# Kernel optimization log

Measured on AMD Instinct MI355X. Metric: run time of the kernel, lower is better.

## Reference

```python
import jax, jax.numpy as jnp
import numpy as np
from jax import lax

COS_BASIS_NO = 24
SCALE = 6.0
SHIFT = 1.0


def make_kern_basis(T_no):
    # [24, T_no] raised-cosine log-time basis, matching the torch loop exactly
    i = jnp.arange(COS_BASIS_NO, dtype=jnp.float32)
    phi = (jnp.pi / 2.0) * i                                  # [24]
    x = jnp.arange(T_no, dtype=jnp.float32)
    raw = SCALE * jnp.log(x + SHIFT + 1e-7)                   # [T_no]
    basis = 0.5 * jnp.cos(raw[None, :] - phi[:, None]) + 0.5  # [24, T_no]
    inside = (raw[None, :] >= phi[:, None] - jnp.pi) & (raw[None, :] <= phi[:, None] + jnp.pi)
    return jnp.where(inside, basis, 0.0)


def causal_grouped_conv(x, kern, sub_no, T_no):
    # x: [B, sub_no, T], kern: [sub_no*hid, T_no] (already flipped like torch)
    # left-pad T_no-1 zeros == the torch zero-padded buffer; cross-correlation
    rhs = kern[:, None, :]  # OIH with I=1 per group
    return lax.conv_general_dilated(
        x, rhs, window_strides=(1,), padding=[(T_no - 1, 0)],
        feature_group_count=sub_no,
        dimension_numbers=("NCH", "OIH", "NCH"))


def setup_inputs() -> dict:
    key = jax.random.key(0)
    ks = jax.random.split(key, 10)
    B, T_data = 8, 5000
    sub_no, E_no, I_no, T_no, hid_no = 20, 2000, 200, 400, 16
    inp = {
        "S_e": jax.random.uniform(ks[0], (B, T_data, E_no), dtype=jnp.float32),
        "S_i": jax.random.uniform(ks[1], (B, T_data, I_no), dtype=jnp.float32),
        "E_scale": jnp.zeros((E_no,), jnp.float32),
        "I_scale": jnp.zeros((I_no,), jnp.float32),
        "W_e_layer1": jax.random.normal(ks[2], (sub_no * hid_no, COS_BASIS_NO), jnp.float32) * 0.01,
        "W_i_layer1": jax.random.normal(ks[3], (sub_no * hid_no, COS_BASIS_NO), jnp.float32) * 0.01,
        "W_layer2": jnp.full((sub_no, hid_no), -1.0, jnp.float32),
        "b_layer1": jnp.zeros((sub_no * hid_no,), jnp.float32),
        "C_syn_e_raw": jax.random.normal(ks[4], (sub_no, E_no), jnp.float32) * 0.01,
        "C_syn_i_raw": jax.random.normal(ks[5], (sub_no, I_no), jnp.float32) * 0.01,
        "V_o": jnp.zeros((1,), jnp.float32),
        "temp": jnp.asarray(1.0, jnp.float32),
        "T_no": T_no,
        "test": 1,
    }
    return inp


def reference(S_e, S_i, E_scale, I_scale, W_e_layer1, W_i_layer1, W_layer2,
              b_layer1, C_syn_e_raw, C_syn_i_raw, V_o, temp, T_no, test):
    sub_no = C_syn_e_raw.shape[0]
    hid_no = W_layer2.shape[1]
    B, T_data, _ = S_e.shape

    if test:
        C_syn_e = jax.nn.softmax(C_syn_e_raw / temp, axis=0)
        C_syn_i = jax.nn.softmax(C_syn_i_raw / temp, axis=0)
    else:
        eps = 1e-8
        ku, kv = jax.random.split(jax.random.key(42))
        u_e = jax.random.uniform(ku, C_syn_e_raw.shape, dtype=C_syn_e_raw.dtype)
        u_i = jax.random.uniform(kv, C_syn_i_raw.shape, dtype=C_syn_i_raw.dtype)
        g_e = -jnp.log(-jnp.log(u_e + eps) + eps)
        g_i = -jnp.log(-jnp.log(u_i + eps) + eps)
        C_syn_e = jax.nn.softmax((C_syn_e_raw + g_e) / temp, axis=0)
        C_syn_i = jax.nn.softmax((C_syn_i_raw + g_i) / temp, axis=0)

    # scale synapses and project onto subunits: [B,T,E] x [E,sub] -> [B,T,sub]
    syn_e = jnp.einsum("bte,se->bts", S_e * jnp.exp(E_scale)[None, None, :], C_syn_e)
    syn_i = jnp.einsum("bti,si->bts", S_i * jnp.exp(I_scale)[None, None, :], C_syn_i)

    kern_basis = make_kern_basis(T_no)                        # [24, T_no]
    ke = jnp.flip(W_e_layer1 @ kern_basis, axis=1)            # [sub*hid, T_no]
    ki = jnp.flip(W_i_layer1 @ kern_basis, axis=1)

    xe = jnp.transpose(syn_e, (0, 2, 1))                      # [B, sub, T]
    xi = jnp.transpose(syn_i, (0, 2, 1))
    conv_e = causal_grouped_conv(xe, ke, sub_no, T_no)        # [B, sub*hid, T]
    conv_i = causal_grouped_conv(xi, ki, sub_no, T_no)
    layer1 = jnp.tanh(conv_e + conv_i + b_layer1[None, :, None])

    # grouped 1x1 conv == per-subunit weighted reduction over hid
    h = layer1.reshape(B, sub_no, hid_no, T_data)
    sub_out = jnp.einsum("bshT,sh->bTs", h, jnp.exp(W_layer2))  # [B, T, sub]
    final = jnp.sum(sub_out, axis=-1) + V_o                    # [B, T]
    return final, sub_out, C_syn_e, C_syn_i
```

## Files before the change

kernel.cpp:

```cpp
#include <hip/hip_runtime.h>
#include <math.h>

#define PI_F 3.14159265358979323846f
#define BSTRIDE 404

__global__ __launch_bounds__(256) void prep_kernel(
    const float* __restrict__ Ce_raw, const float* __restrict__ Ci_raw,
    const float* __restrict__ Escale, const float* __restrict__ Iscale,
    const float* __restrict__ temp,
    float* __restrict__ CsT_e, float* __restrict__ CsT_i,
    float* __restrict__ basis,
    float* __restrict__ outCe, float* __restrict__ outCi)
{
    int id = blockIdx.x * 256 + threadIdx.x;
    if (id < 2000) {
        int e = id;
        float t = temp[0];
        float v[20];
        float m = -1e30f;
        #pragma unroll
        for (int s = 0; s < 20; ++s) { v[s] = Ce_raw[s * 2000 + e] / t; m = fmaxf(m, v[s]); }
        float sum = 0.f;
        #pragma unroll
        for (int s = 0; s < 20; ++s) { v[s] = expf(v[s] - m); sum += v[s]; }
        float inv = 1.f / sum;
        float sc = expf(Escale[e]);
        #pragma unroll
        for (int s = 0; s < 20; ++s) {
            float p = v[s] * inv;
            outCe[s * 2000 + e] = p;
            CsT_e[e * 20 + s] = p * sc;
        }
    } else if (id < 2200) {
        int e = id - 2000;
        float t = temp[0];
        float v[20];
        float m = -1e30f;
        #pragma unroll
        for (int s = 0; s < 20; ++s) { v[s] = Ci_raw[s * 200 + e] / t; m = fmaxf(m, v[s]); }
        float sum = 0.f;
        #pragma unroll
        for (int s = 0; s < 20; ++s) { v[s] = expf(v[s] - m); sum += v[s]; }
        float inv = 1.f / sum;
        float sc = expf(Iscale[e]);
        #pragma unroll
        for (int s = 0; s < 20; ++s) {
            float p = v[s] * inv;
            outCi[s * 200 + e] = p;
            CsT_i[e * 20 + s] = p * sc;
        }
    } else if (id < 2200 + 24 * BSTRIDE) {
        int idx = id - 2200;
        int j = idx / BSTRIDE, d = idx - j * BSTRIDE;
        float val = 0.f;
        if (d < 400) {
            float raw = 6.0f * logf((float)d + 1.0f + 1e-7f);
            float ph = (PI_F * 0.5f) * (float)j;
            if (raw >= ph - PI_F && raw <= ph + PI_F) val = 0.5f * cosf(raw - ph) + 0.5f;
        }
        basis[idx] = val;
    } else if (id < 11896 + 48) {
        int row = 2000 + (id - 11896);
        #pragma unroll
        for (int s = 0; s < 20; ++s) CsT_e[row * 20 + s] = 0.f;
    } else if (id < 11944 + 56) {
        int row = 200 + (id - 11944);
        #pragma unroll
        for (int s = 0; s < 20; ++s) CsT_i[row * 20 + s] = 0.f;
    }
}

template <int NCHUNK>
__global__ __launch_bounds__(256) void syn_kernel(
    const float* __restrict__ S, const float* __restrict__ CsT,
    float* __restrict__ syn, int Eno)
{
    __shared__ float4 tile[64 * 33];
    float* red = reinterpret_cast<float*>(tile);
    const int tid = threadIdx.x;
    const int lane = tid & 63;
    const int w = __builtin_amdgcn_readfirstlane(tid >> 6);
    const int r0 = blockIdx.x * 64;

    float acc[20];
    #pragma unroll
    for (int s = 0; s < 20; ++s) acc[s] = 0.f;

    const int frow = tid >> 5, fcol = tid & 31;

    auto issue = [&](int ch, float4 (&v)[8]) {
        const int ebase = ch * 128;
        #pragma unroll
        for (int i = 0; i < 8; ++i) {
            int row = frow + i * 8;
            int e0 = ebase + fcol * 4;
            v[i] = make_float4(0.f, 0.f, 0.f, 0.f);
            if (e0 + 4 <= Eno)
                v[i] = *reinterpret_cast<const float4*>(S + (size_t)(r0 + row) * Eno + e0);
        }
    };
    auto put = [&](float4 (&v)[8]) {
        #pragma unroll
        for (int i = 0; i < 8; ++i)
            tile[(frow + i * 8) * 33 + fcol] = v[i];
    };

    float4 nx[8];
    issue(0, nx);
    put(nx);

    for (int ch = 0; ch < NCHUNK; ++ch) {
        __syncthreads();
        if (ch + 1 < NCHUNK) issue(ch + 1, nx);

        const int ebase = ch * 128;
        const float4* crow = reinterpret_cast<const float4*>(CsT + (size_t)(ebase + w * 32) * 20);
        #pragma unroll
        for (int c4 = 0; c4 < 8; ++c4) {
            float4 v = tile[lane * 33 + w * 8 + c4];
            const float4* ct = crow + c4 * 20;
            float vv[4] = {v.x, v.y, v.z, v.w};
            #pragma unroll
            for (int q = 0; q < 4; ++q) {
                float sv = vv[q];
                #pragma unroll
                for (int c5 = 0; c5 < 5; ++c5) {
                    float4 cc = ct[q * 5 + c5];
                    acc[c5 * 4 + 0] = fmaf(sv, cc.x, acc[c5 * 4 + 0]);
                    acc[c5 * 4 + 1] = fmaf(sv, cc.y, acc[c5 * 4 + 1]);
                    acc[c5 * 4 + 2] = fmaf(sv, cc.z, acc[c5 * 4 + 2]);
                    acc[c5 * 4 + 3] = fmaf(sv, cc.w, acc[c5 * 4 + 3]);
                }
            }
        }
        __syncthreads();
        if (ch + 1 < NCHUNK) put(nx);
    }

    #pragma unroll
    for (int s = 0; s < 20; ++s) red[(w * 64 + lane) * 21 + s] = acc[s];
    __syncthreads();

    #pragma unroll
    for (int i = 0; i < 5; ++i) {
        int p = tid + i * 256;
        int row = p & 63, s = p >> 6;
        float a = red[(0 * 64 + row) * 21 + s] + red[(1 * 64 + row) * 21 + s]
                + red[(2 * 64 + row) * 21 + s] + red[(3 * 64 + row) * 21 + s];
        int r = r0 + row;
        int b = r / 5000, t = r - b * 5000;
        syn[((size_t)b * 20 + s) * 5000 + t] = a;
    }
}

__device__ const int CJ_LO[24] = {0,0,0,0,0,0,0,0,0,4,4,8,12,16,20,28,36,48,64,84,108,140,184,240};
__device__ const int CJ_NB[24] = {1,1,1,1,2,2,3,3,4,4,5,6,7,9,12,15,19,25,31,41,53,65,54,40};

__device__ __forceinline__ int phys4(int g) {
    return (g & ~15) | ((g >> 1) & 7) | ((g & 1) << 3);
}

__global__ __launch_bounds__(128) void conv_kernel(
    const float* __restrict__ syn_e, const float* __restrict__ syn_i,
    const float* __restrict__ basis,
    const float* __restrict__ W_e, const float* __restrict__ W_i,
    const float* __restrict__ b1, const float* __restrict__ W2,
    float* __restrict__ sub_out)
{
    __shared__ float4 win4[16 + 464];
    float4* wbase = win4 + 16;
    float2* win2 = reinterpret_cast<float2*>(wbase);
    const int tid = threadIdx.x;
    const int tile = blockIdx.x, s = blockIdx.y, bz = blockIdx.z;
    const int t0 = tile * 512;

    const float* se = syn_e + ((size_t)bz * 20 + s) * 5000;
    const float* si = syn_i + ((size_t)bz * 20 + s) * 5000;
    for (int l = tid; l < 920; l += 128) {
        int t = t0 - 404 + l;
        float ve = 0.f, vi = 0.f;
        if ((unsigned)t < 5000u) { ve = se[t]; vi = si[t]; }
        int g = l >> 1;
        win2[2 * phys4(g) + (l & 1)] = make_float2(ve, vi);
    }
    __syncthreads();

    float z[16][4];
    #pragma unroll
    for (int h = 0; h < 16; ++h) {
        float bv = b1[s * 16 + h];
        #pragma unroll
        for (int k = 0; k < 4; ++k) z[h][k] = bv;
    }

    const int base = 4 * tid + 400;

    for (int j = 0; j < 24; ++j) {
        const float4* bj4 = reinterpret_cast<const float4*>(basis + j * BSTRIDE);
        const int lo = CJ_LO[j];
        const int nb = CJ_NB[j];
        const int co = lo >> 2;
        float be0 = 0.f, be1 = 0.f, be2 = 0.f, be3 = 0.f;
        float bi0 = 0.f, bi1 = 0.f, bi2 = 0.f, bi3 = 0.f;

        auto body = [&](const float4& V0, const float4& V1,
                        const float4& V2, const float4& V3, const float4& c) {
            be0 = fmaf(c.x, V2.x, be0); bi0 = fmaf(c.x, V2.y, bi0);
            be1 = fmaf(c.x, V2.z, be1); bi1 = fmaf(c.x, V2.w, bi1);
            be2 = fmaf(c.x, V3.x, be2); bi2 = fmaf(c.x, V3.y, bi2);
            be3 = fmaf(c.x, V3.z, be3); bi3 = fmaf(c.x, V3.w, bi3);
            be0 = fmaf(c.y, V1.z, be0); bi0 = fmaf(c.y, V1.w, bi0);
            be1 = fmaf(c.y, V2.x, be1); bi1 = fmaf(c.y, V2.y, bi1);
            be2 = fmaf(c.y, V2.z, be2); bi2 = fmaf(c.y, V2.w, bi2);
            be3 = fmaf(c.y, V3.x, be3); bi3 = fmaf(c.y, V3.y, bi3);
            be0 = fmaf(c.z, V1.x, be0); bi0 = fmaf(c.z, V1.y, bi0);
            be1 = fmaf(c.z, V1.z, be1); bi1 = fmaf(c.z, V1.w, bi1);
            be2 = fmaf(c.z, V2.x, be2); bi2 = fmaf(c.z, V2.y, bi2);
            be3 = fmaf(c.z, V2.z, be3); bi3 = fmaf(c.z, V2.w, bi3);
            be0 = fmaf(c.w, V0.z, be0); bi0 = fmaf(c.w, V0.w, bi0);
            be1 = fmaf(c.w, V1.x, be1); bi1 = fmaf(c.w, V1.y, bi1);
            be2 = fmaf(c.w, V1.z, be2); bi2 = fmaf(c.w, V1.w, bi2);
            be3 = fmaf(c.w, V2.x, be3); bi3 = fmaf(c.w, V2.y, bi3);
        };

        const int g0 = (base - lo) >> 1;
        auto LP = [&](int n, float4& lo4, float4& hi4) {
            int p = phys4(g0 - 2 * n);
            lo4 = wbase[p]; hi4 = wbase[p + 8];
        };

        float4 A0, A1, B0, B1, C0, C1, D0, D1;
        float4 E0, E1, F0, F1, G0, G1, H0, H1;
        LP(-1, A0, A1); LP(0, B0, B1); LP(1, C0, C1); LP(2, D0, D1);
        float4 cB = bj4[co], cC = bj4[co + 1], cD = bj4[co + 2];

        int bb = 0;
        while (bb + 8 <= nb) {
            LP(bb + 3, E0, E1); float4 cE = bj4[co + bb + 3];
            body(B0, B1, A0, A1, cB);
            LP(bb + 4, F0, F1); float4 cF = bj4[co + bb + 4];
            body(C0, C1, B0, B1, cC);
            LP(bb + 5, G0, G1); float4 cG = bj4[co + bb + 5];
            body(D0, D1, C0, C1, cD);
            LP(bb + 6, H0, H1); float4 cH = bj4[co + bb + 6];
            body(E0, E1, D0, D1, cE);
            LP(bb + 7, A0, A1); float4 cI = bj4[co + bb + 7];
            body(F0, F1, E0, E1, cF);
            LP(bb + 8, B0, B1); cB = bj4[co + bb + 8];
            body(G0, G1, F0, F1, cG);
            LP(bb + 9, C0, C1); cC = bj4[co + bb + 9];
            body(H0, H1, G0, G1, cH);
            LP(bb + 10, D0, D1); cD = bj4[co + bb + 10];
            body(A0, A1, H0, H1, cI);
            bb += 8;
        }
        int r = nb - bb;
        if (r > 0) { body(B0, B1, A0, A1, cB);
          if (r > 1) { body(C0, C1, B0, B1, cC);
            if (r > 2) { body(D0, D1, C0, C1, cD);
              if (r > 3) { LP(bb + 3, E0, E1); float4 cE = bj4[co + bb + 3];
                body(E0, E1, D0, D1, cE);
                if (r > 4) { LP(bb + 4, F0, F1); float4 cF = bj4[co + bb + 4];
                  body(F0, F1, E0, E1, cF);
                  if (r > 5) { LP(bb + 5, G0, G1); float4 cG = bj4[co + bb + 5];
                    body(G0, G1, F0, F1, cG);
                    if (r > 6) { LP(bb + 6, H0, H1); float4 cH = bj4[co + bb + 6];
                      body(H0, H1, G0, G1, cH); } } } } } } }

        #pragma unroll
        for (int h = 0; h < 16; ++h) {
            float we = W_e[(s * 16 + h) * 24 + j];
            float wi = W_i[(s * 16 + h) * 24 + j];
            z[h][0] = fmaf(we, be0, fmaf(wi, bi0, z[h][0]));
            z[h][1] = fmaf(we, be1, fmaf(wi, bi1, z[h][1]));
            z[h][2] = fmaf(we, be2, fmaf(wi, bi2, z[h][2]));
            z[h][3] = fmaf(we, be3, fmaf(wi, bi3, z[h][3]));
        }
    }

    float w2v[16];
    #pragma unroll
    for (int h = 0; h < 16; ++h) w2v[h] = __expf(W2[s * 16 + h]);

    #pragma unroll
    for (int k = 0; k < 4; ++k) {
        int t = t0 + 4 * tid + k;
        if (t < 5000) {
            float acc = 0.f;
            #pragma unroll
            for (int h = 0; h < 16; ++h) {
                float e2 = __expf(2.0f * z[h][k]);
                float th = 1.0f - 2.0f / (e2 + 1.0f);
                acc = fmaf(w2v[h], th, acc);
            }
            sub_out[((size_t)bz * 5000 + t) * 20 + s] = acc;
        }
    }
}

__global__ __launch_bounds__(256) void final_kernel(
    const float* __restrict__ sub_out, const float* __restrict__ V_o,
    float* __restrict__ fin)
{
    int r = blockIdx.x * 256 + threadIdx.x;
    if (r < 40000) {
        const float* p = sub_out + (size_t)r * 20;
        float a = V_o[0];
        #pragma unroll
        for (int s = 0; s < 20; ++s) a += p[s];
        fin[r] = a;
    }
}

extern "C" void kernel_launch(void* const* d_in, const int* in_sizes, int n_in,
                              void* d_out, int out_size, void* d_ws, size_t ws_size,
                              hipStream_t stream)
{
    const float* S_e     = (const float*)d_in[0];
    const float* S_i     = (const float*)d_in[1];
    const float* E_scale = (const float*)d_in[2];
    const float* I_scale = (const float*)d_in[3];
    const float* W_e     = (const float*)d_in[4];
    const float* W_i     = (const float*)d_in[5];
    const float* W2      = (const float*)d_in[6];
    const float* b1      = (const float*)d_in[7];
    const float* Ce_raw  = (const float*)d_in[8];
    const float* Ci_raw  = (const float*)d_in[9];
    const float* V_o     = (const float*)d_in[10];
    const float* temp    = (const float*)d_in[11];

    float* out     = (float*)d_out;
    float* fin     = out;
    float* sub_out = out + 40000;
    float* outCe   = out + 840000;
    float* outCi   = out + 880000;

    float* ws    = (float*)d_ws;
    float* CsT_e = ws;
    float* CsT_i = ws + 40960;
    float* basis = ws + 46080;
    float* syn_e = ws + 55776;
    float* syn_i = ws + 855776;

    prep_kernel<<<47, 256, 0, stream>>>(Ce_raw, Ci_raw, E_scale, I_scale, temp,
                                        CsT_e, CsT_i, basis, outCe, outCi);
    syn_kernel<16><<<625, 256, 0, stream>>>(S_e, CsT_e, syn_e, 2000);
    syn_kernel<2><<<625, 256, 0, stream>>>(S_i, CsT_i, syn_i, 200);
    conv_kernel<<<dim3(10, 20, 8), 128, 0, stream>>>(syn_e, syn_i, basis,
                                                     W_e, W_i, b1, W2, sub_out);
    final_kernel<<<157, 256, 0, stream>>>(sub_out, V_o, fin);
}
```

Baseline: 292.6 us.

## Restructure synapse projection as per-wave 4-row dot products with blocked coefficient layout

The synapse projection kernel no longer stages S tiles through shared memory with block-wide syncs. Each wave now handles 4 time rows: lanes stride over the input dimension and read coalesced scalars of S, then finish with a shuffle reduction across the wave. The prep kernel writes the softmax coefficients in a lane-interleaved float4 layout so each lane loads its 20 coefficients with vector loads. This drops the LDS traffic and barriers, at the cost of 80 accumulators per thread, a 6-step shuffle reduction per output, and scalar rather than float4 global loads of S.

```diff
diff --git a/kernel.cpp b/kernel.cpp
--- a/kernel.cpp
+++ b/kernel.cpp
@@ -8,7 +8,7 @@
     const float* __restrict__ Ce_raw, const float* __restrict__ Ci_raw,
     const float* __restrict__ Escale, const float* __restrict__ Iscale,
     const float* __restrict__ temp,
-    float* __restrict__ CsT_e, float* __restrict__ CsT_i,
+    float4* __restrict__ CbE, float4* __restrict__ CbI,
     float* __restrict__ basis,
     float* __restrict__ outCe, float* __restrict__ outCi)
 {
@@ -25,11 +25,16 @@
         for (int s = 0; s < 20; ++s) { v[s] = expf(v[s] - m); sum += v[s]; }
         float inv = 1.f / sum;
         float sc = expf(Escale[e]);
-        #pragma unroll
-        for (int s = 0; s < 20; ++s) {
-            float p = v[s] * inv;
-            outCe[s * 2000 + e] = p;
-            CsT_e[e * 20 + s] = p * sc;
+        int bi = (e >> 6) * 5, ln = e & 63;
+        #pragma unroll
+        for (int s4 = 0; s4 < 5; ++s4) {
+            float p0 = v[s4*4+0] * inv, p1 = v[s4*4+1] * inv;
+            float p2 = v[s4*4+2] * inv, p3 = v[s4*4+3] * inv;
+            outCe[(s4*4+0) * 2000 + e] = p0;
+            outCe[(s4*4+1) * 2000 + e] = p1;
+            outCe[(s4*4+2) * 2000 + e] = p2;
+            outCe[(s4*4+3) * 2000 + e] = p3;
+            CbE[(bi + s4) * 64 + ln] = make_float4(p0*sc, p1*sc, p2*sc, p3*sc);
         }
     } else if (id < 2200) {
         int e = id - 2000;
@@ -43,11 +48,16 @@
         for (int s = 0; s < 20; ++s) { v[s] = expf(v[s] - m); sum += v[s]; }
         float inv = 1.f / sum;
         float sc = expf(Iscale[e]);
-        #pragma unroll
-        for (int s = 0; s < 20; ++s) {
-            float p = v[s] * inv;
-            outCi[s * 200 + e] = p;
-            CsT_i[e * 20 + s] = p * sc;
+        int bi = (e >> 6) * 5, ln = e & 63;
+        #pragma unroll
+        for (int s4 = 0; s4 < 5; ++s4) {
+            float p0 = v[s4*4+0] * inv, p1 = v[s4*4+1] * inv;
+            float p2 = v[s4*4+2] * inv, p3 = v[s4*4+3] * inv;
+            outCi[(s4*4+0) * 200 + e] = p0;
+            outCi[(s4*4+1) * 200 + e] = p1;
+            outCi[(s4*4+2) * 200 + e] = p2;
+            outCi[(s4*4+3) * 200 + e] = p3;
+            CbI[(bi + s4) * 64 + ln] = make_float4(p0*sc, p1*sc, p2*sc, p3*sc);
         }
     } else if (id < 2200 + 24 * BSTRIDE) {
         int idx = id - 2200;
@@ -60,96 +70,107 @@
         }
         basis[idx] = val;
     } else if (id < 11896 + 48) {
-        int row = 2000 + (id - 11896);
-        #pragma unroll
-        for (int s = 0; s < 20; ++s) CsT_e[row * 20 + s] = 0.f;
+        int e = 2000 + (id - 11896);
+        int bi = (e >> 6) * 5, ln = e & 63;
+        #pragma unroll
+        for (int s4 = 0; s4 < 5; ++s4)
+            CbE[(bi + s4) * 64 + ln] = make_float4(0.f, 0.f, 0.f, 0.f);
     } else if (id < 11944 + 56) {
-        int row = 200 + (id - 11944);
-        #pragma unroll
-        for (int s = 0; s < 20; ++s) CsT_i[row * 20 + s] = 0.f;
-    }
-}
-
-template <int NCHUNK>
+        int e = 200 + (id - 11944);
+        int bi = (e >> 6) * 5, ln = e & 63;
+        #pragma unroll
+        for (int s4 = 0; s4 < 5; ++s4)
+            CbI[(bi + s4) * 64 + ln] = make_float4(0.f, 0.f, 0.f, 0.f);
+    }
+}
+
+template <int NFULL>
 __global__ __launch_bounds__(256) void syn_kernel(
-    const float* __restrict__ S, const float* __restrict__ CsT,
+    const float* __restrict__ S, const float4* __restrict__ Cb,
     float* __restrict__ syn, int Eno)
 {
-    __shared__ float4 tile[64 * 33];
-    float* red = reinterpret_cast<float*>(tile);
-    const int tid = threadIdx.x;
-    const int lane = tid & 63;
-    const int w = __builtin_amdgcn_readfirstlane(tid >> 6);
-    const int r0 = blockIdx.x * 64;
-
-    float acc[20];
-    #pragma unroll
-    for (int s = 0; s < 20; ++s) acc[s] = 0.f;
-
-    const int frow = tid >> 5, fcol = tid & 31;
-
-    auto issue = [&](int ch, float4 (&v)[8]) {
-        const int ebase = ch * 128;
-        #pragma unroll
-        for (int i = 0; i < 8; ++i) {
-            int row = frow + i * 8;
-            int e0 = ebase + fcol * 4;
-            v[i] = make_float4(0.f, 0.f, 0.f, 0.f);
-            if (e0 + 4 <= Eno)
-                v[i] = *reinterpret_cast<const float4*>(S + (size_t)(r0 + row) * Eno + e0);
-        }
-    };
-    auto put = [&](float4 (&v)[8]) {
-        #pragma unroll
-        for (int i = 0; i < 8; ++i)
-            tile[(frow + i * 8) * 33 + fcol] = v[i];
-    };
-
-    float4 nx[8];
-    issue(0, nx);
-    put(nx);
-
-    for (int ch = 0; ch < NCHUNK; ++ch) {
-        __syncthreads();
-        if (ch + 1 < NCHUNK) issue(ch + 1, nx);
-
-        const int ebase = ch * 128;
-        const float4* crow = reinterpret_cast<const float4*>(CsT + (size_t)(ebase + w * 32) * 20);
-        #pragma unroll
-        for (int c4 = 0; c4 < 8; ++c4) {
-            float4 v = tile[lane * 33 + w * 8 + c4];
-            const float4* ct = crow + c4 * 20;
-            float vv[4] = {v.x, v.y, v.z, v.w};
+    const int lane = threadIdx.x & 63;
+    const int gw = blockIdx.x * 4 + (threadIdx.x >> 6);
+    const int r0 = gw * 4;
+    const size_t sb = (size_t)r0 * Eno;
+
+    float acc[4][20];
+    #pragma unroll
+    for (int m = 0; m < 4; ++m)
+        #pragma unroll
+        for (int s = 0; s < 20; ++s) acc[m][s] = 0.f;
+
+    const float4* cbl = Cb + lane;
+
+    #pragma unroll 2
+    for (int eb = 0; eb < NFULL; ++eb) {
+        const int e = eb * 64 + lane;
+        float sv[4];
+        sv[0] = S[sb + e];
+        sv[1] = S[sb + (size_t)Eno + e];
+        sv[2] = S[sb + (size_t)(2 * Eno) + e];
+        sv[3] = S[sb + (size_t)(3 * Eno) + e];
+        float4 c[5];
+        #pragma unroll
+        for (int s4 = 0; s4 < 5; ++s4) c[s4] = cbl[(eb * 5 + s4) * 64];
+        #pragma unroll
+        for (int m = 0; m < 4; ++m) {
+            float s_ = sv[m];
             #pragma unroll
-            for (int q = 0; q < 4; ++q) {
-                float sv = vv[q];
-                #pragma unroll
-                for (int c5 = 0; c5 < 5; ++c5) {
-                    float4 cc = ct[q * 5 + c5];
-                    acc[c5 * 4 + 0] = fmaf(sv, cc.x, acc[c5 * 4 + 0]);
-                    acc[c5 * 4 + 1] = fmaf(sv, cc.y, acc[c5 * 4 + 1]);
-                    acc[c5 * 4 + 2] = fmaf(sv, cc.z, acc[c5 * 4 + 2]);
-                    acc[c5 * 4 + 3] = fmaf(sv, cc.w, acc[c5 * 4 + 3]);
-                }
+            for (int s4 = 0; s4 < 5; ++s4) {
+                acc[m][s4*4+0] = fmaf(s_, c[s4].x, acc[m][s4*4+0]);
+                acc[m][s4*4+1] = fmaf(s_, c[s4].y, acc[m][s4*4+1]);
+                acc[m][s4*4+2] = fmaf(s_, c[s4].z, acc[m][s4*4+2]);
+                acc[m][s4*4+3] = fmaf(s_, c[s4].w, acc[m][s4*4+3]);
             }
         }
-        __syncthreads();
-        if (ch + 1 < NCHUNK) put(nx);
-    }
-
-    #pragma unroll
-    for (int s = 0; s < 20; ++s) red[(w * 64 + lane) * 21 + s] = acc[s];
-    __syncthreads();
-
-    #pragma unroll
-    for (int i = 0; i < 5; ++i) {
-        int p = tid + i * 256;
-        int row = p & 63, s = p >> 6;
-        float a = red[(0 * 64 + row) * 21 + s] + red[(1 * 64 + row) * 21 + s]
-                + red[(2 * 64 + row) * 21 + s] + red[(3 * 64 + row) * 21 + s];
-        int r = r0 + row;
-        int b = r / 5000, t = r - b * 5000;
-        syn[((size_t)b * 20 + s) * 5000 + t] = a;
+    }
+    {
+        const int e = NFULL * 64 + lane;
+        const bool ok = e < Eno;
+        float sv[4];
+        sv[0] = ok ? S[sb + e] : 0.f;
+        sv[1] = ok ? S[sb + (size_t)Eno + e] : 0.f;
+        sv[2] = ok ? S[sb + (size_t)(2 * Eno) + e] : 0.f;
+        sv[3] = ok ? S[sb + (size_t)(3 * Eno) + e] : 0.f;
+        float4 c[5];
+        #pragma unroll
+        for (int s4 = 0; s4 < 5; ++s4) c[s4] = cbl[(NFULL * 5 + s4) * 64];
+        #pragma unroll
+        for (int m = 0; m < 4; ++m) {
+            float s_ = sv[m];
+            #pragma unroll
+            for (int s4 = 0; s4 < 5; ++s4) {
+                acc[m][s4*4+0] = fmaf(s_, c[s4].x, acc[m][s4*4+0]);
+                acc[m][s4*4+1] = fmaf(s_, c[s4].y, acc[m][s4*4+1]);
+                acc[m][s4*4+2] = fmaf(s_, c[s4].z, acc[m][s4*4+2]);
+                acc[m][s4*4+3] = fmaf(s_, c[s4].w, acc[m][s4*4+3]);
+            }
+        }
+    }
+
+    #pragma unroll
+    for (int m = 0; m < 4; ++m)
+        #pragma unroll
+        for (int s = 0; s < 20; ++s) {
+            float v = acc[m][s];
+            v += __shfl_xor(v, 32);
+            v += __shfl_xor(v, 16);
+            v += __shfl_xor(v, 8);
+            v += __shfl_xor(v, 4);
+            v += __shfl_xor(v, 2);
+            v += __shfl_xor(v, 1);
+            acc[m][s] = v;
+        }
+
+    if (lane == 0) {
+        const int b = r0 / 5000;
+        const int t = r0 - b * 5000;
+        #pragma unroll
+        for (int m = 0; m < 4; ++m)
+            #pragma unroll
+            for (int s = 0; s < 20; ++s)
+                syn[((size_t)b * 20 + s) * 5000 + t + m] = acc[m][s];
     }
 }
 
@@ -336,16 +357,16 @@
     float* outCi   = out + 880000;
 
     float* ws    = (float*)d_ws;
-    float* CsT_e = ws;
-    float* CsT_i = ws + 40960;
+    float4* CbE  = (float4*)ws;
+    float4* CbI  = (float4*)(ws + 40960);
     float* basis = ws + 46080;
     float* syn_e = ws + 55776;
     float* syn_i = ws + 855776;
 
     prep_kernel<<<47, 256, 0, stream>>>(Ce_raw, Ci_raw, E_scale, I_scale, temp,
-                                        CsT_e, CsT_i, basis, outCe, outCi);
-    syn_kernel<16><<<625, 256, 0, stream>>>(S_e, CsT_e, syn_e, 2000);
-    syn_kernel<2><<<625, 256, 0, stream>>>(S_i, CsT_i, syn_i, 200);
+                                        CbE, CbI, basis, outCe, outCi);
+    syn_kernel<31><<<2500, 256, 0, stream>>>(S_e, CbE, syn_e, 2000);
+    syn_kernel<3><<<2500, 256, 0, stream>>>(S_i, CbI, syn_i, 200);
     conv_kernel<<<dim3(10, 20, 8), 128, 0, stream>>>(syn_e, syn_i, basis,
                                                      W_e, W_i, b1, W2, sub_out);
     final_kernel<<<157, 256, 0, stream>>>(sub_out, V_o, fin);
```

Result: slower. 371.5 us (+27.0%).
